# Kernel tuning notes

Measured on AMD Instinct MI355X. Metric: run time of the kernel, lower is better.

## Reference

```python
import jax, jax.numpy as jnp
import numpy as np

B, S, D = 2, 1024, 1024
H, KV, HD = 16, 4, 64
E, F = 8, 3584
EPS = 1e-5
TOP_K = 2


def setup_inputs() -> dict:
    key = jax.random.key(0)
    ks = jax.random.split(key, 12)
    sc = 0.02
    inv_freq = 1.0 / (10000.0 ** (np.arange(0, HD, 2, dtype=np.float32) / HD))
    freqs = np.outer(np.arange(S, dtype=np.float32), inv_freq)
    emb = np.concatenate([freqs, freqs], axis=-1)  # [S, HD]
    return {
        'x': jax.random.normal(ks[0], (B, S, D), jnp.float32),
        'ln1_w': jnp.ones((D,), jnp.float32),
        'ln2_w': jnp.ones((D,), jnp.float32),
        'wq': jax.random.normal(ks[1], (H * HD, D), jnp.float32) * sc,
        'wk': jax.random.normal(ks[2], (KV * HD, D), jnp.float32) * sc,
        'wv': jax.random.normal(ks[3], (KV * HD, D), jnp.float32) * sc,
        'wo': jax.random.normal(ks[4], (D, H * HD), jnp.float32) * sc,
        'gate_w': jax.random.normal(ks[5], (E, D), jnp.float32) * sc,
        'w1': jax.random.normal(ks[6], (E, F, D), jnp.float32) * sc,
        'w2': jax.random.normal(ks[7], (E, D, F), jnp.float32) * sc,
        'w3': jax.random.normal(ks[8], (E, F, D), jnp.float32) * sc,
        'cos': jnp.asarray(np.cos(emb)),
        'sin': jnp.asarray(np.sin(emb)),
    }


def _rms_norm(x, w):
    var = jnp.mean(jnp.square(x), axis=-1, keepdims=True)
    return x * jax.lax.rsqrt(var + EPS) * w


def _rotate_half(x):
    x1, x2 = jnp.split(x, 2, axis=-1)
    return jnp.concatenate([-x2, x1], axis=-1)


def _attn(h, wq, wk, wv, wo, cos, sin):
    # h: [B,S,D]
    q = (h @ wq.T).reshape(B, S, H, HD).transpose(0, 2, 1, 3)      # [B,H,S,HD]
    k = (h @ wk.T).reshape(B, S, KV, HD).transpose(0, 2, 1, 3)     # [B,KV,S,HD]
    v = (h @ wv.T).reshape(B, S, KV, HD).transpose(0, 2, 1, 3)
    c = cos[None, None, :S, :]
    s = sin[None, None, :S, :]
    q = q * c + _rotate_half(q) * s
    k = k * c + _rotate_half(k) * s
    k = jnp.repeat(k, H // KV, axis=1)  # GQA expand -> [B,H,S,HD]
    v = jnp.repeat(v, H // KV, axis=1)
    scores = jnp.einsum('bhqd,bhkd->bhqk', q, k) / jnp.sqrt(jnp.float32(HD))
    causal = jnp.tril(jnp.ones((S, S), bool))
    scores = jnp.where(causal[None, None], scores, jnp.float32(-1e30))
    probs = jax.nn.softmax(scores, axis=-1)
    out = jnp.einsum('bhqk,bhkd->bhqd', probs, v)
    out = out.transpose(0, 2, 1, 3).reshape(B, S, H * HD)
    return out @ wo.T


def _moe(h, gate_w, w1, w2, w3):
    T = B * S
    hs = h.reshape(T, D)
    probs = jax.nn.softmax(hs @ gate_w.T, axis=-1)       # [T,E]
    _, sel = jax.lax.top_k(probs, TOP_K)                  # [T,2]
    rw = jnp.take_along_axis(probs, sel, axis=-1)
    rw = rw / jnp.sum(rw, axis=-1, keepdims=True)
    cw = jnp.zeros((T, E), hs.dtype).at[jnp.arange(T)[:, None], sel].add(rw)  # [T,E] combine weights
    h1 = jnp.einsum('td,efd->tef', hs, w1)               # [T,E,F]
    h3 = jnp.einsum('td,efd->tef', hs, w3)
    inter = jax.nn.silu(h1) * h3
    out = jnp.einsum('tef,edf,te->td', inter, w2, cw)
    return out.reshape(B, S, D)


def reference(x, ln1_w, ln2_w, wq, wk, wv, wo, gate_w, w1, w2, w3, cos, sin):
    h = x + _attn(_rms_norm(x, ln1_w), wq, wk, wv, wo, cos, sin)
    h = h + _moe(_rms_norm(h, ln2_w), gate_w, w1, w2, w3)
    return h
```

## Files before the change

### kernel.cpp

```cpp
#include <hip/hip_runtime.h>

typedef unsigned short u16;
using short8 = __attribute__((ext_vector_type(8))) short;
using f32x4  = __attribute__((ext_vector_type(4))) float;

#define TQ   2048
#define DM   1024
#define SLEN 1024
#define FDIM 3584
#define NEXP 8

static __device__ __forceinline__ u16 f2bf(float f) {
  union { float f; unsigned u; } a; a.f = f;
  unsigned r = a.u + 0x7fffu + ((a.u >> 16) & 1u);
  return (u16)(r >> 16);
}
static __device__ __forceinline__ float bf2f(u16 u) {
  union { unsigned u; float f; } a; a.u = ((unsigned)u) << 16;
  return a.f;
}
static __device__ __forceinline__ unsigned cvtpk(float lo, float hi) {
  unsigned r;
  asm volatile("v_cvt_pk_bf16_f32 %0, %1, %2" : "=v"(r) : "v"(lo), "v"(hi));
  return r;
}

static __device__ __forceinline__ void gload16(const void* g, void* l) {
  __builtin_amdgcn_global_load_lds((const __attribute__((address_space(1))) void*)g,
                                   (__attribute__((address_space(3))) void*)l, 16, 0, 0);
}

static __device__ __forceinline__ int xcd_lid(int bid, int cpx) {
  return (bid & 7) * cpx + (bid >> 3);
}

static __device__ __forceinline__ void cvtwr8(float4 a, float4 b, u16* dst) {
  uint4 u;
  u.x = cvtpk(a.x, a.y); u.y = cvtpk(a.z, a.w);
  u.z = cvtpk(b.x, b.y); u.w = cvtpk(b.z, b.w);
  *(uint4*)dst = u;
}

__global__ __launch_bounds__(256) void rmsnorm_kernel(
    const float* __restrict__ x, const float* __restrict__ w,
    u16* __restrict__ oh, u16* __restrict__ ol, float* __restrict__ of) {
  int t = blockIdx.x, tid = threadIdx.x;
  const float4* xr = (const float4*)(x + (size_t)t * DM);
  float4 v = xr[tid];
  float ss = v.x * v.x + v.y * v.y + v.z * v.z + v.w * v.w;
#pragma unroll
  for (int m = 1; m < 64; m <<= 1) ss += __shfl_xor(ss, m);
  __shared__ float red[4];
  if ((tid & 63) == 0) red[tid >> 6] = ss;
  __syncthreads();
  float tot = red[0] + red[1] + red[2] + red[3];
  float sc = rsqrtf(tot * (1.0f / DM) + 1e-5f);
  float4 wv = ((const float4*)w)[tid];
  float o0 = v.x * sc * wv.x, o1 = v.y * sc * wv.y, o2 = v.z * sc * wv.z, o3 = v.w * sc * wv.w;
  ushort4 hh;
  hh.x = f2bf(o0); hh.y = f2bf(o1); hh.z = f2bf(o2); hh.w = f2bf(o3);
  *(ushort4*)(oh + (size_t)t * DM + tid * 4) = hh;
  if (ol) {
    ushort4 ll;
    ll.x = f2bf(o0 - bf2f(hh.x)); ll.y = f2bf(o1 - bf2f(hh.y));
    ll.z = f2bf(o2 - bf2f(hh.z)); ll.w = f2bf(o3 - bf2f(hh.w));
    *(ushort4*)(ol + (size_t)t * DM + tid * 4) = ll;
  }
  if (of) {
    float4 o4; o4.x = o0; o4.y = o1; o4.z = o2; o4.w = o3;
    ((float4*)(of + (size_t)t * DM))[tid] = o4;
  }
}

__global__ __launch_bounds__(256) void wconv_split_kernel(
    const float* __restrict__ wq, const float* __restrict__ wk,
    const float* __restrict__ wv, const float* __restrict__ wo,
    u16* __restrict__ qkvh, u16* __restrict__ qkvl,
    u16* __restrict__ woh, u16* __restrict__ wol) {
  for (int i = blockIdx.x * 256 + threadIdx.x; i < 655360; i += 640 * 256) {
    int el = i * 4;
    const float* src; u16 *dh, *dl;
    if (el < 1572864) {
      int r = el >> 10, c = el & 1023;
      if (r < 1024) src = wq + el;
      else if (r < 1280) src = wk + (r - 1024) * 1024 + c;
      else src = wv + (r - 1280) * 1024 + c;
      dh = qkvh + el; dl = qkvl + el;
    } else {
      int e2 = el - 1572864;
      src = wo + e2; dh = woh + e2; dl = wol + e2;
    }
    float4 v = *(const float4*)src;
    ushort4 h, l;
    h.x = f2bf(v.x); h.y = f2bf(v.y); h.z = f2bf(v.z); h.w = f2bf(v.w);
    l.x = f2bf(v.x - bf2f(h.x)); l.y = f2bf(v.y - bf2f(h.y));
    l.z = f2bf(v.z - bf2f(h.z)); l.w = f2bf(v.w - bf2f(h.w));
    *(ushort4*)dh = h; *(ushort4*)dl = l;
  }
}

template <bool RESID>
__global__ __launch_bounds__(256) void gemm_split2_kernel(
    const u16* __restrict__ Ah, const u16* __restrict__ Al,
    const u16* __restrict__ Wh, const u16* __restrict__ Wl,
    float* __restrict__ C, const float* __restrict__ resid, int N, int cpx) {
  __shared__ u16 sAh[2][128][32], sAl[2][128][32], sWh[2][64][32], sWl[2][64][32];
  int lid = xcd_lid(blockIdx.x, cpx);
  int bm = lid & 15, bn = lid >> 4;
  int tid = threadIdx.x, lane = tid & 63, w = tid >> 6;
  int wm = w >> 1, wn = w & 1;
  int qi = lane & 15, g = lane >> 4;
  int lr = lane >> 2, lc = (lane & 3) * 8;
  const u16* pa0 = Ah + (size_t)(bm * 128 + w * 16 + lr) * DM + lc;
  const u16* pa1 = pa0 + 64 * DM;
  const u16* pl0 = Al + (size_t)(bm * 128 + w * 16 + lr) * DM + lc;
  const u16* pl1 = pl0 + 64 * DM;
  const u16* pw  = Wh + (size_t)(bn * 64 + w * 16 + lr) * DM + lc;
  const u16* pwl = Wl + (size_t)(bn * 64 + w * 16 + lr) * DM + lc;
  f32x4 acc[4][2] = {};
#define STG2(buf, kk) do { \
    gload16(pa0 + (kk), &sAh[buf][w * 16][0]); \
    gload16(pa1 + (kk), &sAh[buf][64 + w * 16][0]); \
    gload16(pl0 + (kk), &sAl[buf][w * 16][0]); \
    gload16(pl1 + (kk), &sAl[buf][64 + w * 16][0]); \
    gload16(pw  + (kk), &sWh[buf][w * 16][0]); \
    gload16(pwl + (kk), &sWl[buf][w * 16][0]); } while (0)
  STG2(0, 0);
  asm volatile("s_waitcnt vmcnt(0)" ::: "memory");
  __syncthreads();
  for (int ks = 0; ks < 32; ks++) {
    int cur = ks & 1;
    if (ks < 31) STG2(cur ^ 1, (ks + 1) * 32);
    short8 afh[4], afl[4], bfh[2], bfl[2];
#pragma unroll
    for (int i = 0; i < 4; i++) {
      afh[i] = *(short8*)&sAh[cur][wm * 64 + i * 16 + qi][g * 8];
      afl[i] = *(short8*)&sAl[cur][wm * 64 + i * 16 + qi][g * 8];
    }
#pragma unroll
    for (int i = 0; i < 2; i++) {
      bfh[i] = *(short8*)&sWh[cur][wn * 32 + i * 16 + qi][g * 8];
      bfl[i] = *(short8*)&sWl[cur][wn * 32 + i * 16 + qi][g * 8];
    }
#pragma unroll
    for (int mi = 0; mi < 4; mi++)
#pragma unroll
      for (int ni = 0; ni < 2; ni++) {
        f32x4 a = acc[mi][ni];
        a = __builtin_amdgcn_mfma_f32_16x16x32_bf16(afh[mi], bfh[ni], a, 0, 0, 0);
        a = __builtin_amdgcn_mfma_f32_16x16x32_bf16(afl[mi], bfh[ni], a, 0, 0, 0);
        a = __builtin_amdgcn_mfma_f32_16x16x32_bf16(afh[mi], bfl[ni], a, 0, 0, 0);
        acc[mi][ni] = a;
      }
    asm volatile("s_waitcnt vmcnt(0)" ::: "memory");
    __syncthreads();
  }
#undef STG2
#pragma unroll
  for (int mi = 0; mi < 4; mi++)
#pragma unroll
    for (int ni = 0; ni < 2; ni++) {
      int col = bn * 64 + wn * 32 + ni * 16 + qi;
#pragma unroll
      for (int r = 0; r < 4; r++) {
        int row = bm * 128 + wm * 64 + mi * 16 + g * 4 + r;
        float val = acc[mi][ni][r];
        if (RESID) val += resid[(size_t)row * N + col];
        C[(size_t)row * N + col] = val;
      }
    }
}

__global__ __launch_bounds__(256) void rope_split_kernel(
    const float* __restrict__ qkvf,
    const float* __restrict__ cosT, const float* __restrict__ sinT,
    u16* __restrict__ qh, u16* __restrict__ ql, u16* __restrict__ kh, u16* __restrict__ kl,
    u16* __restrict__ vh, u16* __restrict__ vl) {
  int t = blockIdx.x, tid = threadIdx.x;
  int s = t & (SLEN - 1);
  const float* rowp = qkvf + (size_t)t * 1536;
#pragma unroll
  for (int it = 0; it < 2; it++) {
    int i = it * 256 + tid;
    int hh = i >> 5, d = i & 31;
    float c = cosT[s * 64 + d], sn = sinT[s * 64 + d];
    size_t dst = (size_t)t * DM + hh * 64 + d;
    float x1 = rowp[hh * 64 + d], x2 = rowp[hh * 64 + d + 32];
    float o1 = x1 * c - x2 * sn;
    float o2 = x2 * c + x1 * sn;
    u16 h1 = f2bf(o1), h2 = f2bf(o2);
    qh[dst] = h1; qh[dst + 32] = h2;
    ql[dst] = f2bf(o1 - bf2f(h1)); ql[dst + 32] = f2bf(o2 - bf2f(h2));
  }
  if (tid < 128) {
    int hh = tid >> 5, d = tid & 31;
    float c = cosT[s * 64 + d], sn = sinT[s * 64 + d];
    size_t dst = (size_t)t * 256 + hh * 64 + d;
    float x1 = rowp[1024 + hh * 64 + d], x2 = rowp[1024 + hh * 64 + d + 32];
    float o1 = x1 * c - x2 * sn;
    float o2 = x2 * c + x1 * sn;
    u16 h1 = f2bf(o1), h2 = f2bf(o2);
    kh[dst] = h1; kh[dst + 32] = h2;
    kl[dst] = f2bf(o1 - bf2f(h1)); kl[dst + 32] = f2bf(o2 - bf2f(h2));
  }
  {
    size_t dst = (size_t)t * 256 + tid;
    float v = rowp[1280 + tid];
    u16 h = f2bf(v);
    vh[dst] = h; vl[dst] = f2bf(v - bf2f(h));
  }
}

__global__ __launch_bounds__(256) void attn_kernel(
    const u16* __restrict__ qh, const u16* __restrict__ ql,
    const u16* __restrict__ kh, const u16* __restrict__ kl,
    const u16* __restrict__ vh, const u16* __restrict__ vl,
    u16* __restrict__ oh, u16* __restrict__ ol) {
  __shared__ u16 sKh[64][72], sKl[64][72];
  __shared__ u16 sVh[64][72], sVl[64][72];
  __shared__ u16 sPh[4][16][72], sPl[4][16][72];
  int p = blockIdx.x & 7;
  int bh = blockIdx.x >> 3;
  int b = bh >> 4, h = bh & 15, kvh = h >> 2;
  int tid = threadIdx.x, lane = tid & 63, w = tid >> 6;
  int qi = lane & 15, g = lane >> 4;
#pragma unroll
  for (int half = 0; half < 2; half++) {
    int qt = half ? (15 - p) : p;
    int qrow = qt * 64 + w * 16 + qi;
    size_t qbase = ((size_t)(b * SLEN + qrow)) * DM + h * 64;
    short8 qfh[2], qfl[2];
#pragma unroll
    for (int ds = 0; ds < 2; ds++) {
      qfh[ds] = *(const short8*)(qh + qbase + ds * 32 + g * 8);
      qfl[ds] = *(const short8*)(ql + qbase + ds * 32 + g * 8);
    }
    f32x4 oacc[4] = {};
    float mrun = -1e30f, lrun = 0.f;
    int ktiles = qt + 1;
    for (int kt = 0; kt < ktiles; kt++) {
      __syncthreads();
      {
        int r = tid >> 3, cs = (tid & 7) * 8;
#pragma unroll
        for (int rr = 0; rr < 64; rr += 32) {
          int key = kt * 64 + rr + r;
          size_t src = ((size_t)(b * SLEN + key)) * 256 + kvh * 64 + cs;
          *(short8*)&sKh[rr + r][cs] = *(const short8*)(kh + src);
          *(short8*)&sKl[rr + r][cs] = *(const short8*)(kl + src);
          short8 vv = *(const short8*)(vh + src);
          short8 vv2 = *(const short8*)(vl + src);
#pragma unroll
          for (int j = 0; j < 8; j++) {
            sVh[cs + j][rr + r] = (u16)vv[j];
            sVl[cs + j][rr + r] = (u16)vv2[j];
          }
        }
      }
      __syncthreads();
      f32x4 sa[4];
#pragma unroll
      for (int kf = 0; kf < 4; kf++) {
        f32x4 a = {};
#pragma unroll
        for (int ds = 0; ds < 2; ds++) {
          short8 kfh = *(short8*)&sKh[kf * 16 + qi][ds * 32 + g * 8];
          short8 kfl = *(short8*)&sKl[kf * 16 + qi][ds * 32 + g * 8];
          a = __builtin_amdgcn_mfma_f32_16x16x32_bf16(kfh, qfh[ds], a, 0, 0, 0);
          a = __builtin_amdgcn_mfma_f32_16x16x32_bf16(kfl, qfh[ds], a, 0, 0, 0);
          a = __builtin_amdgcn_mfma_f32_16x16x32_bf16(kfh, qfl[ds], a, 0, 0, 0);
        }
        sa[kf] = a;
      }
      int qg = qt * 64 + w * 16 + qi;
      float sv[4][4];
      float tmax = -1e30f;
#pragma unroll
      for (int kf = 0; kf < 4; kf++)
#pragma unroll
        for (int r = 0; r < 4; r++) {
          int key = kt * 64 + kf * 16 + g * 4 + r;
          float s = sa[kf][r] * 0.125f;
          s = (key <= qg) ? s : -1e30f;
          sv[kf][r] = s;
          tmax = fmaxf(tmax, s);
        }
      tmax = fmaxf(tmax, __shfl_xor(tmax, 16));
      tmax = fmaxf(tmax, __shfl_xor(tmax, 32));
      float mn = fmaxf(mrun, tmax);
      float alpha = expf(mrun - mn);
      float psum = 0.f;
#pragma unroll
      for (int kf = 0; kf < 4; kf++) {
        float p0 = expf(sv[kf][0] - mn), p1 = expf(sv[kf][1] - mn);
        float p2 = expf(sv[kf][2] - mn), p3 = expf(sv[kf][3] - mn);
        psum += p0 + p1 + p2 + p3;
        ushort4 ph, pl;
        ph.x = f2bf(p0); ph.y = f2bf(p1); ph.z = f2bf(p2); ph.w = f2bf(p3);
        pl.x = f2bf(p0 - bf2f(ph.x)); pl.y = f2bf(p1 - bf2f(ph.y));
        pl.z = f2bf(p2 - bf2f(ph.z)); pl.w = f2bf(p3 - bf2f(ph.w));
        *(ushort4*)&sPh[w][qi][kf * 16 + g * 4] = ph;
        *(ushort4*)&sPl[w][qi][kf * 16 + g * 4] = pl;
      }
      psum += __shfl_xor(psum, 16);
      psum += __shfl_xor(psum, 32);
      lrun = lrun * alpha + psum;
      mrun = mn;
#pragma unroll
      for (int df = 0; df < 4; df++) {
        oacc[df][0] *= alpha; oacc[df][1] *= alpha;
        oacc[df][2] *= alpha; oacc[df][3] *= alpha;
      }
#pragma unroll
      for (int ks = 0; ks < 2; ks++) {
        short8 pfh = *(short8*)&sPh[w][qi][ks * 32 + g * 8];
        short8 pfl = *(short8*)&sPl[w][qi][ks * 32 + g * 8];
#pragma unroll
        for (int df = 0; df < 4; df++) {
          short8 vfh = *(short8*)&sVh[df * 16 + qi][ks * 32 + g * 8];
          short8 vfl = *(short8*)&sVl[df * 16 + qi][ks * 32 + g * 8];
          f32x4 a = oacc[df];
          a = __builtin_amdgcn_mfma_f32_16x16x32_bf16(vfh, pfh, a, 0, 0, 0);
          a = __builtin_amdgcn_mfma_f32_16x16x32_bf16(vfl, pfh, a, 0, 0, 0);
          a = __builtin_amdgcn_mfma_f32_16x16x32_bf16(vfh, pfl, a, 0, 0, 0);
          oacc[df] = a;
        }
      }
    }
    float inv = 1.0f / lrun;
    size_t obase = ((size_t)(b * SLEN + qt * 64 + w * 16 + qi)) * DM + h * 64;
#pragma unroll
    for (int df = 0; df < 4; df++) {
      float o0 = oacc[df][0] * inv, o1 = oacc[df][1] * inv;
      float o2 = oacc[df][2] * inv, o3 = oacc[df][3] * inv;
      ushort4 hh, ll;
      hh.x = f2bf(o0); hh.y = f2bf(o1); hh.z = f2bf(o2); hh.w = f2bf(o3);
      ll.x = f2bf(o0 - bf2f(hh.x)); ll.y = f2bf(o1 - bf2f(hh.y));
      ll.z = f2bf(o2 - bf2f(hh.z)); ll.w = f2bf(o3 - bf2f(hh.w));
      *(ushort4*)(oh + obase + df * 16 + g * 4) = hh;
      *(ushort4*)(ol + obase + df * 16 + g * 4) = ll;
    }
  }
}

__global__ void zero8_kernel(int* p) { if (threadIdx.x < 8) p[threadIdx.x] = 0; }

__global__ __launch_bounds__(64) void gate_kernel(
    const float* __restrict__ hf, const float* __restrict__ gw,
    int* cnt, int* tok_e, int* tok_pos, float* tok_w) {
  int t = blockIdx.x, lane = threadIdx.x;
  float acc[8] = {0, 0, 0, 0, 0, 0, 0, 0};
  for (int i = lane; i < DM; i += 64) {
    float h = hf[(size_t)t * DM + i];
#pragma unroll
    for (int e = 0; e < 8; e++) acc[e] += h * gw[e * DM + i];
  }
#pragma unroll
  for (int e = 0; e < 8; e++)
#pragma unroll
    for (int m = 1; m < 64; m <<= 1) acc[e] += __shfl_xor(acc[e], m);
  if (lane == 0) {
    int i0 = 0;
#pragma unroll
    for (int e = 1; e < 8; e++) if (acc[e] > acc[i0]) i0 = e;
    int i1 = -1;
#pragma unroll
    for (int e = 0; e < 8; e++) if (e != i0 && (i1 < 0 || acc[e] > acc[i1])) i1 = e;
    float w0 = 1.0f;
    float w1 = expf(acc[i1] - acc[i0]);
    float rs = 1.0f / (w0 + w1);
    int p0 = atomicAdd(&cnt[i0], 1);
    int p1 = atomicAdd(&cnt[i1], 1);
    tok_e[t * 2] = i0; tok_e[t * 2 + 1] = i1;
    tok_pos[t * 2] = p0; tok_pos[t * 2 + 1] = p1;
    tok_w[t * 2] = w0 * rs; tok_w[t * 2 + 1] = w1 * rs;
  }
}

__global__ void schedule_kernel(const int* cnt, int* offs, int* mt,
                                int* row_e, int* row_bm) {
  if (threadIdx.x == 0) {
    int s = 0, m = 0;
    for (int e = 0; e < 8; e++) {
      offs[e] = s;
      int nb = (cnt[e] + 127) >> 7;
      for (int i = 0; i < nb; i++) { row_e[m] = e; row_bm[m] = i; m++; }
      s += cnt[e];
    }
    *mt = m;
  }
}

__global__ __launch_bounds__(256) void gather_kernel(
    const u16* __restrict__ hn2b, const int* __restrict__ tok_e,
    const int* __restrict__ tok_pos, const float* __restrict__ tok_w,
    const int* __restrict__ offs, u16* __restrict__ Xg,
    int* __restrict__ pair_tok, int* __restrict__ pair_slot, float* __restrict__ pair_w) {
  int t = blockIdx.x;
#pragma unroll
  for (int slot = 0; slot < 2; slot++) {
    int e = tok_e[t * 2 + slot];
    int p = offs[e] + tok_pos[t * 2 + slot];
    ((ushort4*)(Xg + (size_t)p * DM))[threadIdx.x] =
        ((const ushort4*)(hn2b + (size_t)t * DM))[threadIdx.x];
    if (threadIdx.x == 0) {
      pair_tok[p] = t; pair_slot[p] = slot; pair_w[p] = tok_w[t * 2 + slot];
    }
  }
}

__global__ __launch_bounds__(256) void moe_gemm13_kernel(
    const u16* __restrict__ Xg, const float* __restrict__ w1,
    const float* __restrict__ w3, const int* __restrict__ cnt,
    const int* __restrict__ offs, const int* __restrict__ mt,
    const int* __restrict__ row_e, const int* __restrict__ row_bm,
    u16* __restrict__ inter) {
  __shared__ u16 sA[3][128][32];
  __shared__ u16 sW1[3][64][32], sW3[3][64][32];
  int MT = *mt;
  int active = MT * 56;
  int cpx = (active + 7) >> 3;
  int xg8 = blockIdx.x >> 3;
  if (xg8 >= cpx) return;
  int lid = (blockIdx.x & 7) * cpx + xg8;
  if (lid >= active) return;
  int mrow = lid % MT, bn = lid / MT;
  int e = row_e[mrow], bm = row_bm[mrow];
  int count = cnt[e], off = offs[e];
  const u16* A = Xg + (size_t)off * DM;
  const float* W1 = w1 + (size_t)e * FDIM * DM;
  const float* W3 = w3 + (size_t)e * FDIM * DM;
  int tid = threadIdx.x, lane = tid & 63, w = tid >> 6;
  int wm = w >> 1, wn = w & 1;
  int qi = lane & 15, g = lane >> 4;
  int lrA = lane >> 2, lcA = (lane & 3) * 8;
  int ga0 = bm * 128 + w * 32 + lrA;      if (ga0 >= count) ga0 = count - 1;
  int ga1 = bm * 128 + w * 32 + 16 + lrA; if (ga1 >= count) ga1 = count - 1;
  const u16* pa0 = A + (size_t)ga0 * DM + lcA;
  const u16* pa1 = A + (size_t)ga1 * DM + lcA;
  int r16 = lane >> 2;
  int rW = w * 16 + r16;
  int cW = (lane & 3) * 8;
  const float* q1 = W1 + (size_t)(bn * 64 + rW) * DM + cW;
  const float* q3 = W3 + (size_t)(bn * 64 + rW) * DM + cW;
  int uW = ((lane & 3) ^ (r16 & 3)) * 8;
  f32x4 acc1[4][2] = {}, acc3[4][2] = {};
  float4 p1a = *(const float4*)q1, p1b = *(const float4*)(q1 + 4);
  float4 p3a = *(const float4*)q3, p3b = *(const float4*)(q3 + 4);
  float4 v1a = *(const float4*)(q1 + 32), v1b = *(const float4*)(q1 + 36);
  float4 v3a = *(const float4*)(q3 + 32), v3b = *(const float4*)(q3 + 36);
  __builtin_amdgcn_sched_barrier(0);
  gload16(pa0, &sA[0][w * 32][0]);
  gload16(pa1, &sA[0][w * 32 + 16][0]);
  gload16(pa0 + 32, &sA[1][w * 32][0]);
  gload16(pa1 + 32, &sA[1][w * 32 + 16][0]);
  asm volatile("s_waitcnt vmcnt(8)" ::: "memory");
  cvtwr8(p1a, p1b, &sW1[0][rW][uW]);
  cvtwr8(p3a, p3b, &sW3[0][rW][uW]);
  for (int ks = 0; ks < 32; ks++) {
    int cur = ks % 3;
    if (ks == 0)       asm volatile("s_waitcnt vmcnt(2) lgkmcnt(0)" ::: "memory");
    else if (ks == 31) asm volatile("s_waitcnt vmcnt(0) lgkmcnt(0)" ::: "memory");
    else               asm volatile("s_waitcnt vmcnt(6) lgkmcnt(0)" ::: "memory");
    __builtin_amdgcn_s_barrier();
    short8 af[4], b1[2], b3[2];
#pragma unroll
    for (int i = 0; i < 4; i++)
      af[i] = *(short8*)&sA[cur][wm * 64 + i * 16 + qi][g * 8];
#pragma unroll
    for (int ni = 0; ni < 2; ni++) {
      int rt = wn * 32 + ni * 16 + qi;
      int ui = (g ^ (rt & 3)) * 8;
      b1[ni] = *(short8*)&sW1[cur][rt][ui];
      b3[ni] = *(short8*)&sW3[cur][rt][ui];
    }
    __builtin_amdgcn_s_setprio(1);
#pragma unroll
    for (int mi = 0; mi < 4; mi++)
#pragma unroll
      for (int ni = 0; ni < 2; ni++) {
        acc1[mi][ni] = __builtin_amdgcn_mfma_f32_16x16x32_bf16(af[mi], b1[ni], acc1[mi][ni], 0, 0, 0);
        acc3[mi][ni] = __builtin_amdgcn_mfma_f32_16x16x32_bf16(af[mi], b3[ni], acc3[mi][ni], 0, 0, 0);
      }
    __builtin_amdgcn_s_setprio(0);
    if (ks < 31) {
      int nb = (ks + 1) % 3;
      cvtwr8(v1a, v1b, &sW1[nb][rW][uW]);
      cvtwr8(v3a, v3b, &sW3[nb][rW][uW]);
      if (ks < 30) {
        int k2 = (ks + 2) * 32;
        v1a = *(const float4*)(q1 + k2); v1b = *(const float4*)(q1 + k2 + 4);
        v3a = *(const float4*)(q3 + k2); v3b = *(const float4*)(q3 + k2 + 4);
        __builtin_amdgcn_sched_barrier(0);
        int ab = (ks + 2) % 3;
        gload16(pa0 + k2, &sA[ab][w * 32][0]);
        gload16(pa1 + k2, &sA[ab][w * 32 + 16][0]);
      }
    }
  }
#pragma unroll
  for (int mi = 0; mi < 4; mi++)
#pragma unroll
    for (int r = 0; r < 4; r++) {
      int row = bm * 128 + wm * 64 + mi * 16 + g * 4 + r;
      if (row < count) {
        size_t obase = (size_t)(off + row) * FDIM + bn * 64 + wn * 32;
#pragma unroll
        for (int ni = 0; ni < 2; ni++) {
          float c1 = acc1[mi][ni][r], c3 = acc3[mi][ni][r];
          float sv = c1 / (1.0f + expf(-c1)) * c3;
          inter[obase + ni * 16 + qi] = f2bf(sv);
        }
      }
    }
}

__global__ __launch_bounds__(256) void moe_gemm2_kernel(
    const u16* __restrict__ inter, const float* __restrict__ w2,
    const int* __restrict__ cnt, const int* __restrict__ offs,
    const int* __restrict__ mt, const int* __restrict__ row_e,
    const int* __restrict__ row_bm,
    const int* __restrict__ pair_tok, const int* __restrict__ pair_slot,
    const float* __restrict__ pair_w, float* __restrict__ pout) {
  __shared__ u16 sA[3][128][32];
  __shared__ u16 sW[3][64][32];
  int MT = *mt;
  int active = MT * 16;
  int cpx = (active + 7) >> 3;
  int xg8 = blockIdx.x >> 3;
  if (xg8 >= cpx) return;
  int lid = (blockIdx.x & 7) * cpx + xg8;
  if (lid >= active) return;
  int mrow = lid % MT, bn = lid / MT;
  int e = row_e[mrow], bm = row_bm[mrow];
  int count = cnt[e], off = offs[e];
  const u16* A = inter + (size_t)off * FDIM;
  const float* W = w2 + (size_t)e * DM * FDIM;
  int tid = threadIdx.x, lane = tid & 63, w = tid >> 6;
  int wm = w >> 1, wn = w & 1;
  int qi = lane & 15, g = lane >> 4;
  int lrA = lane >> 2, lcA = (lane & 3) * 8;
  int ga0 = bm * 128 + w * 32 + lrA;      if (ga0 >= count) ga0 = count - 1;
  int ga1 = bm * 128 + w * 32 + 16 + lrA; if (ga1 >= count) ga1 = count - 1;
  const u16* pa0 = A + (size_t)ga0 * FDIM + lcA;
  const u16* pa1 = A + (size_t)ga1 * FDIM + lcA;
  int r16 = lane >> 2;
  int rW = w * 16 + r16;
  int cW = (lane & 3) * 8;
  const float* qw = W + (size_t)(bn * 64 + rW) * FDIM + cW;
  int uW = ((lane & 3) ^ (r16 & 3)) * 8;
  f32x4 acc[4][2] = {};
  const int NK = FDIM / 32;
  float4 ta = *(const float4*)qw, tb = *(const float4*)(qw + 4);
  float4 va = *(const float4*)(qw + 32), vb = *(const float4*)(qw + 36);
  __builtin_amdgcn_sched_barrier(0);
  gload16(pa0, &sA[0][w * 32][0]);
  gload16(pa1, &sA[0][w * 32 + 16][0]);
  gload16(pa0 + 32, &sA[1][w * 32][0]);
  gload16(pa1 + 32, &sA[1][w * 32 + 16][0]);
  asm volatile("s_waitcnt vmcnt(6)" ::: "memory");
  cvtwr8(ta, tb, &sW[0][rW][uW]);
  for (int ks = 0; ks < NK; ks++) {
    int cur = ks % 3;
    if (ks == 0)           asm volatile("s_waitcnt vmcnt(2) lgkmcnt(0)" ::: "memory");
    else if (ks == NK - 1) asm volatile("s_waitcnt vmcnt(0) lgkmcnt(0)" ::: "memory");
    else                   asm volatile("s_waitcnt vmcnt(4) lgkmcnt(0)" ::: "memory");
    __builtin_amdgcn_s_barrier();
    short8 af[4], bfr[2];
#pragma unroll
    for (int i = 0; i < 4; i++)
      af[i] = *(short8*)&sA[cur][wm * 64 + i * 16 + qi][g * 8];
#pragma unroll
    for (int ni = 0; ni < 2; ni++) {
      int rt = wn * 32 + ni * 16 + qi;
      bfr[ni] = *(short8*)&sW[cur][rt][(g ^ (rt & 3)) * 8];
    }
    __builtin_amdgcn_s_setprio(1);
#pragma unroll
    for (int mi = 0; mi < 4; mi++)
#pragma unroll
      for (int ni = 0; ni < 2; ni++)
        acc[mi][ni] = __builtin_amdgcn_mfma_f32_16x16x32_bf16(af[mi], bfr[ni], acc[mi][ni], 0, 0, 0);
    __builtin_amdgcn_s_setprio(0);
    if (ks < NK - 1) {
      int nb = (ks + 1) % 3;
      cvtwr8(va, vb, &sW[nb][rW][uW]);
      if (ks < NK - 2) {
        int k2 = (ks + 2) * 32;
        va = *(const float4*)(qw + k2); vb = *(const float4*)(qw + k2 + 4);
        __builtin_amdgcn_sched_barrier(0);
        int ab = (ks + 2) % 3;
        gload16(pa0 + k2, &sA[ab][w * 32][0]);
        gload16(pa1 + k2, &sA[ab][w * 32 + 16][0]);
      }
    }
  }
#pragma unroll
  for (int mi = 0; mi < 4; mi++)
#pragma unroll
    for (int r = 0; r < 4; r++) {
      int row = bm * 128 + wm * 64 + mi * 16 + g * 4 + r;
      if (row < count) {
        int p = off + row;
        int t = pair_tok[p];
        float wgt = pair_w[p];
        size_t obase = ((size_t)pair_slot[p] * TQ + t) * DM + bn * 64 + wn * 32;
#pragma unroll
        for (int ni = 0; ni < 2; ni++)
          pout[obase + ni * 16 + qi] = acc[mi][ni][r] * wgt;
      }
    }
}

__global__ __launch_bounds__(256) void combine_kernel(
    const float* __restrict__ h, const float* __restrict__ pout, float* __restrict__ out) {
  size_t i = (size_t)blockIdx.x * 256 + threadIdx.x;
  float4 a = ((const float4*)h)[i];
  float4 b0 = ((const float4*)pout)[i];
  float4 b1 = ((const float4*)pout)[i + (size_t)TQ * DM / 4];
  float4 r;
  r.x = a.x + b0.x + b1.x; r.y = a.y + b0.y + b1.y;
  r.z = a.z + b0.z + b1.z; r.w = a.w + b0.w + b1.w;
  ((float4*)out)[i] = r;
}

extern "C" void kernel_launch(void* const* d_in, const int* in_sizes, int n_in,
                              void* d_out, int out_size, void* d_ws, size_t ws_size,
                              hipStream_t stream) {
  (void)in_sizes; (void)n_in; (void)out_size; (void)ws_size;
  const float* x    = (const float*)d_in[0];
  const float* ln1  = (const float*)d_in[1];
  const float* ln2  = (const float*)d_in[2];
  const float* wq   = (const float*)d_in[3];
  const float* wk   = (const float*)d_in[4];
  const float* wv   = (const float*)d_in[5];
  const float* wo   = (const float*)d_in[6];
  const float* gw   = (const float*)d_in[7];
  const float* w1   = (const float*)d_in[8];
  const float* w2   = (const float*)d_in[9];
  const float* w3   = (const float*)d_in[10];
  const float* cosT = (const float*)d_in[11];
  const float* sinT = (const float*)d_in[12];

  char* mb = (char*)d_ws;
  const size_t MB = 1024 * 1024;
  u16*   qhb  = (u16*)(mb + 0 * MB);
  u16*   qlb  = (u16*)(mb + 4 * MB);
  u16*   khb  = (u16*)(mb + 8 * MB);
  u16*   klb  = (u16*)(mb + 9 * MB);
  u16*   vhb  = (u16*)(mb + 10 * MB);
  u16*   vlb  = (u16*)(mb + 11 * MB);
  u16*   hn2b = (u16*)(mb + 0 * MB);
  float* hn2f = (float*)(mb + 4 * MB);
  u16*   ahb  = (u16*)(mb + 12 * MB);
  u16*   alb  = (u16*)(mb + 16 * MB);
  u16*   Xg   = (u16*)(mb + 12 * MB);
  u16*   hn1h = (u16*)(mb + 20 * MB);
  u16*   hn1l = (u16*)(mb + 24 * MB);
  u16*   inter= (u16*)(mb + 20 * MB);
  float* qkvf = (float*)(mb + 28 * MB);
  float* h_res= (float*)(mb + 48 * MB);
  u16*   woh  = (u16*)(mb + 56 * MB);
  u16*   wol  = (u16*)(mb + 58 * MB);
  float* pout = (float*)(mb + 56 * MB);
  u16*   wqkvh= (u16*)(mb + 60 * MB);
  u16*   wqkvl= (u16*)(mb + 63 * MB);
  int*   cnt  = (int*)(mb + 72 * MB);
  int*   offs = cnt + 8;
  int*   mtp  = cnt + 16;
  int*   row_e  = cnt + 17;
  int*   row_bm = cnt + 57;
  int*   tok_e  = cnt + 128;
  int*   tok_pos = tok_e + 4096;
  float* tok_w   = (float*)(tok_pos + 4096);
  int*   pair_tok  = (int*)(tok_w + 4096);
  int*   pair_slot = pair_tok + 4096;
  float* pair_w    = (float*)(pair_slot + 4096);

  wconv_split_kernel<<<640, 256, 0, stream>>>(wq, wk, wv, wo, wqkvh, wqkvl, woh, wol);
  rmsnorm_kernel<<<TQ, 256, 0, stream>>>(x, ln1, hn1h, hn1l, nullptr);
  gemm_split2_kernel<false><<<384, 256, 0, stream>>>(hn1h, hn1l, wqkvh, wqkvl, qkvf, nullptr, 1536, 48);
  rope_split_kernel<<<TQ, 256, 0, stream>>>(qkvf, cosT, sinT, qhb, qlb, khb, klb, vhb, vlb);
  attn_kernel<<<256, 256, 0, stream>>>(qhb, qlb, khb, klb, vhb, vlb, ahb, alb);
  gemm_split2_kernel<true><<<256, 256, 0, stream>>>(ahb, alb, woh, wol, h_res, x, 1024, 32);
  rmsnorm_kernel<<<TQ, 256, 0, stream>>>(h_res, ln2, hn2b, nullptr, hn2f);
  zero8_kernel<<<1, 64, 0, stream>>>(cnt);
  gate_kernel<<<TQ, 64, 0, stream>>>(hn2f, gw, cnt, tok_e, tok_pos, tok_w);
  schedule_kernel<<<1, 64, 0, stream>>>(cnt, offs, mtp, row_e, row_bm);
  gather_kernel<<<TQ, 256, 0, stream>>>(hn2b, tok_e, tok_pos, tok_w, offs, Xg,
                                        pair_tok, pair_slot, pair_w);
  moe_gemm13_kernel<<<2240, 256, 0, stream>>>(Xg, w1, w3, cnt, offs, mtp,
                                              row_e, row_bm, inter);
  moe_gemm2_kernel<<<640, 256, 0, stream>>>(inter, w2, cnt, offs, mtp,
                                            row_e, row_bm,
                                            pair_tok, pair_slot, pair_w, pout);
  combine_kernel<<<TQ, 256, 0, stream>>>(h_res, pout, (float*)d_out);
}
```

Before: 478.2 us.

## Load MoE expert weights directly into MFMA registers, bypassing LDS staging

```diff
diff --git a/kernel.cpp b/kernel.cpp
--- a/kernel.cpp
+++ b/kernel.cpp
@@ -23,6 +23,12 @@
   unsigned r;
   asm volatile("v_cvt_pk_bf16_f32 %0, %1, %2" : "=v"(r) : "v"(lo), "v"(hi));
   return r;
+}
+static __device__ __forceinline__ short8 pk8(float4 a, float4 b) {
+  union { uint4 u; short8 s; } c;
+  c.u.x = cvtpk(a.x, a.y); c.u.y = cvtpk(a.z, a.w);
+  c.u.z = cvtpk(b.x, b.y); c.u.w = cvtpk(b.z, b.w);
+  return c.s;
 }
 
 static __device__ __forceinline__ void gload16(const void* g, void* l) {
@@ -416,7 +422,6 @@
     const int* __restrict__ row_e, const int* __restrict__ row_bm,
     u16* __restrict__ inter) {
   __shared__ u16 sA[3][128][32];
-  __shared__ u16 sW1[3][64][32], sW3[3][64][32];
   int MT = *mt;
   int active = MT * 56;
   int cpx = (active + 7) >> 3;
@@ -438,42 +443,33 @@
   int ga1 = bm * 128 + w * 32 + 16 + lrA; if (ga1 >= count) ga1 = count - 1;
   const u16* pa0 = A + (size_t)ga0 * DM + lcA;
   const u16* pa1 = A + (size_t)ga1 * DM + lcA;
-  int r16 = lane >> 2;
-  int rW = w * 16 + r16;
-  int cW = (lane & 3) * 8;
-  const float* q1 = W1 + (size_t)(bn * 64 + rW) * DM + cW;
-  const float* q3 = W3 + (size_t)(bn * 64 + rW) * DM + cW;
-  int uW = ((lane & 3) ^ (r16 & 3)) * 8;
+  int rt0 = bn * 64 + wn * 32 + qi;
+  const float* w1p0 = W1 + (size_t)rt0 * DM + g * 8;
+  const float* w1p1 = w1p0 + 16 * DM;
+  const float* w3p0 = W3 + (size_t)rt0 * DM + g * 8;
+  const float* w3p1 = w3p0 + 16 * DM;
   f32x4 acc1[4][2] = {}, acc3[4][2] = {};
-  float4 p1a = *(const float4*)q1, p1b = *(const float4*)(q1 + 4);
-  float4 p3a = *(const float4*)q3, p3b = *(const float4*)(q3 + 4);
-  float4 v1a = *(const float4*)(q1 + 32), v1b = *(const float4*)(q1 + 36);
-  float4 v3a = *(const float4*)(q3 + 32), v3b = *(const float4*)(q3 + 36);
-  __builtin_amdgcn_sched_barrier(0);
   gload16(pa0, &sA[0][w * 32][0]);
   gload16(pa1, &sA[0][w * 32 + 16][0]);
   gload16(pa0 + 32, &sA[1][w * 32][0]);
   gload16(pa1 + 32, &sA[1][w * 32 + 16][0]);
-  asm volatile("s_waitcnt vmcnt(8)" ::: "memory");
-  cvtwr8(p1a, p1b, &sW1[0][rW][uW]);
-  cvtwr8(p3a, p3b, &sW3[0][rW][uW]);
+  __builtin_amdgcn_sched_barrier(0);
+  float4 f10a = *(const float4*)w1p0, f10b = *(const float4*)(w1p0 + 4);
+  float4 f11a = *(const float4*)w1p1, f11b = *(const float4*)(w1p1 + 4);
+  float4 f30a = *(const float4*)w3p0, f30b = *(const float4*)(w3p0 + 4);
+  float4 f31a = *(const float4*)w3p1, f31b = *(const float4*)(w3p1 + 4);
   for (int ks = 0; ks < 32; ks++) {
     int cur = ks % 3;
-    if (ks == 0)       asm volatile("s_waitcnt vmcnt(2) lgkmcnt(0)" ::: "memory");
-    else if (ks == 31) asm volatile("s_waitcnt vmcnt(0) lgkmcnt(0)" ::: "memory");
-    else               asm volatile("s_waitcnt vmcnt(6) lgkmcnt(0)" ::: "memory");
+    if (ks == 31) asm volatile("s_waitcnt vmcnt(8)" ::: "memory");
+    else          asm volatile("s_waitcnt vmcnt(10)" ::: "memory");
     __builtin_amdgcn_s_barrier();
-    short8 af[4], b1[2], b3[2];
+    short8 b1[2], b3[2];
+    b1[0] = pk8(f10a, f10b); b1[1] = pk8(f11a, f11b);
+    b3[0] = pk8(f30a, f30b); b3[1] = pk8(f31a, f31b);
+    short8 af[4];
 #pragma unroll
     for (int i = 0; i < 4; i++)
       af[i] = *(short8*)&sA[cur][wm * 64 + i * 16 + qi][g * 8];
-#pragma unroll
-    for (int ni = 0; ni < 2; ni++) {
-      int rt = wn * 32 + ni * 16 + qi;
-      int ui = (g ^ (rt & 3)) * 8;
-      b1[ni] = *(short8*)&sW1[cur][rt][ui];
-      b3[ni] = *(short8*)&sW3[cur][rt][ui];
-    }
     __builtin_amdgcn_s_setprio(1);
 #pragma unroll
     for (int mi = 0; mi < 4; mi++)
@@ -484,14 +480,14 @@
       }
     __builtin_amdgcn_s_setprio(0);
     if (ks < 31) {
-      int nb = (ks + 1) % 3;
-      cvtwr8(v1a, v1b, &sW1[nb][rW][uW]);
-      cvtwr8(v3a, v3b, &sW3[nb][rW][uW]);
+      int kk = (ks + 1) * 32;
+      f10a = *(const float4*)(w1p0 + kk); f10b = *(const float4*)(w1p0 + kk + 4);
+      f11a = *(const float4*)(w1p1 + kk); f11b = *(const float4*)(w1p1 + kk + 4);
+      f30a = *(const float4*)(w3p0 + kk); f30b = *(const float4*)(w3p0 + kk + 4);
+      f31a = *(const float4*)(w3p1 + kk); f31b = *(const float4*)(w3p1 + kk + 4);
+      __builtin_amdgcn_sched_barrier(0);
       if (ks < 30) {
         int k2 = (ks + 2) * 32;
-        v1a = *(const float4*)(q1 + k2); v1b = *(const float4*)(q1 + k2 + 4);
-        v3a = *(const float4*)(q3 + k2); v3b = *(const float4*)(q3 + k2 + 4);
-        __builtin_amdgcn_sched_barrier(0);
         int ab = (ks + 2) % 3;
         gload16(pa0 + k2, &sA[ab][w * 32][0]);
         gload16(pa1 + k2, &sA[ab][w * 32 + 16][0]);
@@ -523,7 +519,6 @@
     const int* __restrict__ pair_tok, const int* __restrict__ pair_slot,
     const float* __restrict__ pair_w, float* __restrict__ pout) {
   __shared__ u16 sA[3][128][32];
-  __shared__ u16 sW[3][64][32];
   int MT = *mt;
   int active = MT * 16;
   int cpx = (active + 7) >> 3;
@@ -544,37 +539,29 @@
   int ga1 = bm * 128 + w * 32 + 16 + lrA; if (ga1 >= count) ga1 = count - 1;
   const u16* pa0 = A + (size_t)ga0 * FDIM + lcA;
   const u16* pa1 = A + (size_t)ga1 * FDIM + lcA;
-  int r16 = lane >> 2;
-  int rW = w * 16 + r16;
-  int cW = (lane & 3) * 8;
-  const float* qw = W + (size_t)(bn * 64 + rW) * FDIM + cW;
-  int uW = ((lane & 3) ^ (r16 & 3)) * 8;
+  int rt0 = bn * 64 + wn * 32 + qi;
+  const float* wp0 = W + (size_t)rt0 * FDIM + g * 8;
+  const float* wp1 = wp0 + 16 * FDIM;
   f32x4 acc[4][2] = {};
   const int NK = FDIM / 32;
-  float4 ta = *(const float4*)qw, tb = *(const float4*)(qw + 4);
-  float4 va = *(const float4*)(qw + 32), vb = *(const float4*)(qw + 36);
-  __builtin_amdgcn_sched_barrier(0);
   gload16(pa0, &sA[0][w * 32][0]);
   gload16(pa1, &sA[0][w * 32 + 16][0]);
   gload16(pa0 + 32, &sA[1][w * 32][0]);
   gload16(pa1 + 32, &sA[1][w * 32 + 16][0]);
-  asm volatile("s_waitcnt vmcnt(6)" ::: "memory");
-  cvtwr8(ta, tb, &sW[0][rW][uW]);
+  __builtin_amdgcn_sched_barrier(0);
+  float4 f0a = *(const float4*)wp0, f0b = *(const float4*)(wp0 + 4);
+  float4 f1a = *(const float4*)wp1, f1b = *(const float4*)(wp1 + 4);
   for (int ks = 0; ks < NK; ks++) {
     int cur = ks % 3;
-    if (ks == 0)           asm volatile("s_waitcnt vmcnt(2) lgkmcnt(0)" ::: "memory");
-    else if (ks == NK - 1) asm volatile("s_waitcnt vmcnt(0) lgkmcnt(0)" ::: "memory");
-    else                   asm volatile("s_waitcnt vmcnt(4) lgkmcnt(0)" ::: "memory");
+    if (ks == NK - 1) asm volatile("s_waitcnt vmcnt(4)" ::: "memory");
+    else              asm volatile("s_waitcnt vmcnt(6)" ::: "memory");
     __builtin_amdgcn_s_barrier();
-    short8 af[4], bfr[2];
+    short8 bfr[2];
+    bfr[0] = pk8(f0a, f0b); bfr[1] = pk8(f1a, f1b);
+    short8 af[4];
 #pragma unroll
     for (int i = 0; i < 4; i++)
       af[i] = *(short8*)&sA[cur][wm * 64 + i * 16 + qi][g * 8];
-#pragma unroll
-    for (int ni = 0; ni < 2; ni++) {
-      int rt = wn * 32 + ni * 16 + qi;
-      bfr[ni] = *(short8*)&sW[cur][rt][(g ^ (rt & 3)) * 8];
-    }
     __builtin_amdgcn_s_setprio(1);
 #pragma unroll
     for (int mi = 0; mi < 4; mi++)
@@ -583,12 +570,12 @@
         acc[mi][ni] = __builtin_amdgcn_mfma_f32_16x16x32_bf16(af[mi], bfr[ni], acc[mi][ni], 0, 0, 0);
     __builtin_amdgcn_s_setprio(0);
     if (ks < NK - 1) {
-      int nb = (ks + 1) % 3;
-      cvtwr8(va, vb, &sW[nb][rW][uW]);
+      int kk = (ks + 1) * 32;
+      f0a = *(const float4*)(wp0 + kk); f0b = *(const float4*)(wp0 + kk + 4);
+      f1a = *(const float4*)(wp1 + kk); f1b = *(const float4*)(wp1 + kk + 4);
+      __builtin_amdgcn_sched_barrier(0);
       if (ks < NK - 2) {
         int k2 = (ks + 2) * 32;
-        va = *(const float4*)(qw + k2); vb = *(const float4*)(qw + k2 + 4);
-        __builtin_amdgcn_sched_barrier(0);
         int ab = (ks + 2) % 3;
         gload16(pa0 + k2, &sA[ab][w * 32][0]);
         gload16(pa1 + k2, &sA[ab][w * 32 + 16][0]);
```

New measurement: 689.8 us. 44.2% more time.
